# Kernel optimization log

Hardware: AMD Instinct MI355X
Metric: run time of the kernel (lower is better)

## Reference

```python
import jax, jax.numpy as jnp
import numpy as np

SEQ, B, I, H = 2048, 64, 512, 512

def setup_inputs() -> dict:
    key = jax.random.key(0)
    k1, k2, k3 = jax.random.split(key, 3)
    return {
        "input": jax.random.normal(k1, (SEQ, B, I), dtype=jnp.float32),
        "hx": jnp.zeros((1, B, H), dtype=jnp.float32),
        "weight_ih": jax.random.normal(k2, (H, I), dtype=jnp.float32) * 0.01,
        "weight_hh": jax.random.normal(k3, (H, H), dtype=jnp.float32) * 0.01,
        "bias_ih": jnp.zeros((H,), dtype=jnp.float32),
        "bias_hh": jnp.zeros((H,), dtype=jnp.float32),
    }

def reference(input, hx, weight_ih, weight_hh, bias_ih, bias_hh):
    # Batch the input-side projection across all timesteps in one GEMM:
    # [S,B,I] @ [I,H] -> [S,B,H]
    x_proj = jnp.einsum('sbi,hi->sbh', input, weight_ih) + bias_ih + bias_hh
    h0 = hx[0]  # [B,H]

    def step(h, xp_t):
        h_new = jnp.tanh(xp_t + h @ weight_hh.T)
        return h_new, h_new

    h_last, outputs = jax.lax.scan(step, h0, x_proj)
    return outputs, h_last[None]
```

## Files before the change

### kernel.cpp

```cpp
#include <hip/hip_runtime.h>
#include <stdint.h>

#define S_LEN 2048
#define B_SZ  64
#define I_SZ  512
#define H_SZ  512

typedef __attribute__((ext_vector_type(8))) short bf16x8;
typedef __attribute__((ext_vector_type(4))) float f32x4;

__device__ __forceinline__ uint16_t f2b(float x) {
    uint32_t u = __float_as_uint(x);
    uint32_t r = (u + 0x7fffu + ((u >> 16) & 1u)) >> 16;
    return (uint16_t)r;
}

__device__ __forceinline__ float tfun(float v) {
    float e = __expf(2.f * v);
    return 1.f - 2.f / (e + 1.f);
}

__global__ void cvt_weights_kernel(const float* __restrict__ wih,
                                   const float* __restrict__ whh,
                                   uint16_t* __restrict__ wihb,
                                   uint16_t* __restrict__ whhb) {
    int i = (blockIdx.x * blockDim.x + threadIdx.x) * 4;
    float4 a = *reinterpret_cast<const float4*>(wih + i);
    float4 b = *reinterpret_cast<const float4*>(whh + i);
    union { uint16_t u[4]; uint2 v; } pa, pb;
    pa.u[0] = f2b(a.x); pa.u[1] = f2b(a.y); pa.u[2] = f2b(a.z); pa.u[3] = f2b(a.w);
    pb.u[0] = f2b(b.x); pb.u[1] = f2b(b.y); pb.u[2] = f2b(b.z); pb.u[3] = f2b(b.w);
    *reinterpret_cast<uint2*>(wihb + i) = pa.v;
    *reinterpret_cast<uint2*>(whhb + i) = pb.v;
}

#define BM 128
#define BN 128
#define BK 32

__launch_bounds__(256)
__global__ void xproj_gemm_kernel(const float* __restrict__ inp,
                                  const uint16_t* __restrict__ wihb,
                                  const float* __restrict__ bih,
                                  const float* __restrict__ bhh,
                                  float* __restrict__ xp)
{
    __shared__ __align__(16) uint16_t Asm[2][BM * BK];
    __shared__ __align__(16) uint16_t Bsm[2][BN * BK];

    const int tid  = threadIdx.x;
    const int lane = tid & 63;
    const int w    = tid >> 6;
    const int wm   = (w >> 1) * 64;
    const int wn   = (w & 1) * 64;
    const int bid  = blockIdx.x;
    const int m0   = (bid >> 2) * BM;
    const int n0   = (bid & 3) * BN;

    const int srow  = tid >> 1;
    const int shalf = (tid & 1) * 16;

    float bsum[4];
#pragma unroll
    for (int nn = 0; nn < 4; ++nn) {
        int col = n0 + wn + nn * 16 + (lane & 15);
        bsum[nn] = bih[col] + bhh[col];
    }

    f32x4 acc[4][4];
#pragma unroll
    for (int mm = 0; mm < 4; ++mm)
#pragma unroll
        for (int nn = 0; nn < 4; ++nn)
            acc[mm][nn] = f32x4{0.f, 0.f, 0.f, 0.f};

    float4 ar[4];
    bf16x8 br[2];

    auto loadA = [&](int kt) {
        const float* g = inp + (size_t)(m0 + srow) * I_SZ + kt * BK + shalf;
#pragma unroll
        for (int q = 0; q < 4; ++q) ar[q] = *reinterpret_cast<const float4*>(g + q * 4);
    };
    auto loadB = [&](int kt) {
        const uint16_t* g = wihb + (size_t)(n0 + srow) * I_SZ + kt * BK + shalf;
        br[0] = *reinterpret_cast<const bf16x8*>(g);
        br[1] = *reinterpret_cast<const bf16x8*>(g + 8);
    };
    auto writeA = [&](int buf) {
        alignas(16) uint16_t tmp[16];
#pragma unroll
        for (int q = 0; q < 4; ++q) {
            tmp[q * 4 + 0] = f2b(ar[q].x); tmp[q * 4 + 1] = f2b(ar[q].y);
            tmp[q * 4 + 2] = f2b(ar[q].z); tmp[q * 4 + 3] = f2b(ar[q].w);
        }
        *reinterpret_cast<bf16x8*>(&Asm[buf][srow * BK + shalf])     = *reinterpret_cast<bf16x8*>(tmp);
        *reinterpret_cast<bf16x8*>(&Asm[buf][srow * BK + shalf + 8]) = *reinterpret_cast<bf16x8*>(tmp + 8);
    };
    auto writeB = [&](int buf) {
        *reinterpret_cast<bf16x8*>(&Bsm[buf][srow * BK + shalf])     = br[0];
        *reinterpret_cast<bf16x8*>(&Bsm[buf][srow * BK + shalf + 8]) = br[1];
    };

    loadA(0); loadB(0); writeA(0); writeB(0);
    __syncthreads();

    for (int kt = 0; kt < I_SZ / BK; ++kt) {
        const int cur = kt & 1;
        const bool more = (kt + 1) < I_SZ / BK;
        if (more) { loadA(kt + 1); loadB(kt + 1); }

        bf16x8 afrag[4], bfrag[4];
#pragma unroll
        for (int mm = 0; mm < 4; ++mm)
            afrag[mm] = *reinterpret_cast<const bf16x8*>(
                &Asm[cur][(wm + mm * 16 + (lane & 15)) * BK + (lane >> 4) * 8]);
#pragma unroll
        for (int nn = 0; nn < 4; ++nn)
            bfrag[nn] = *reinterpret_cast<const bf16x8*>(
                &Bsm[cur][(wn + nn * 16 + (lane & 15)) * BK + (lane >> 4) * 8]);
#pragma unroll
        for (int mm = 0; mm < 4; ++mm)
#pragma unroll
            for (int nn = 0; nn < 4; ++nn)
                acc[mm][nn] = __builtin_amdgcn_mfma_f32_16x16x32_bf16(
                    afrag[mm], bfrag[nn], acc[mm][nn], 0, 0, 0);

        if (more) { writeA(cur ^ 1); writeB(cur ^ 1); }
        __syncthreads();
    }

#pragma unroll
    for (int mm = 0; mm < 4; ++mm) {
        const int rbase = m0 + wm + mm * 16 + (lane >> 4) * 4;
#pragma unroll
        for (int nn = 0; nn < 4; ++nn) {
            const int col = n0 + wn + nn * 16 + (lane & 15);
#pragma unroll
            for (int r = 0; r < 4; ++r)
                xp[(size_t)(rbase + r) * H_SZ + col] = acc[mm][nn][r] + bsum[nn];
        }
    }
}


#define REP16(M) M(0) M(1) M(2) M(3) M(4) M(5) M(6) M(7) \
                 M(8) M(9) M(10) M(11) M(12) M(13) M(14) M(15)

#define LDW(jt, kt) (*reinterpret_cast<const bf16x8*>( \
    whhb + (size_t)(w * 64 + (jt) * 16 + r16) * H_SZ + (kt) * 32 + q * 8))

#define DECLA(k) bf16x8 rA##k, rB##k, rC##k;
#define LOADA(k) { \
    bf16x8 t0 = LDW(0, k), t1 = LDW(1, k), t2 = LDW(2, k); \
    asm("" : "=a"(rA##k) : "0"(t0)); \
    asm("" : "=a"(rB##k) : "0"(t1)); \
    asm("" : "=a"(rC##k) : "0"(t2)); }

#define KSTEP(k) { \
    bf16x8 bf = *reinterpret_cast<const bf16x8*>(hb + (k) * 32 + q * 8); \
    bf16x8 al = *reinterpret_cast<const bf16x8*>(&Asm[(w * 16 + (k)) * 512 + lane * 8]); \
    c0 = __builtin_amdgcn_mfma_f32_16x16x32_bf16(rA##k, bf, c0, 0, 0, 0); \
    c1 = __builtin_amdgcn_mfma_f32_16x16x32_bf16(rB##k, bf, c1, 0, 0, 0); \
    c2 = __builtin_amdgcn_mfma_f32_16x16x32_bf16(rC##k, bf, c2, 0, 0, 0); \
    c3 = __builtin_amdgcn_mfma_f32_16x16x32_bf16(al,   bf, c3, 0, 0, 0); }

#define STEP(P, XP, sidx, CHKLAST)                                                          \
  {                                                                                          \
    const uint16_t* hb = &hsm[P][0];                                                         \
    f32x4 c0{0.f,0.f,0.f,0.f}, c1{0.f,0.f,0.f,0.f}, c2{0.f,0.f,0.f,0.f}, c3{0.f,0.f,0.f,0.f};\
    REP16(KSTEP)                                                                             \
    if (r16 == 0) {                                                                          \
      *reinterpret_cast<f32x4*>(&ysm[w * 64 +  0 + q * 4]) = c0;                             \
      *reinterpret_cast<f32x4*>(&ysm[w * 64 + 16 + q * 4]) = c1;                             \
      *reinterpret_cast<f32x4*>(&ysm[w * 64 + 32 + q * 4]) = c2;                             \
      *reinterpret_cast<f32x4*>(&ysm[w * 64 + 48 + q * 4]) = c3;                             \
    }                                                                                        \
    asm volatile("s_waitcnt lgkmcnt(0)" ::: "memory");                                       \
    __builtin_amdgcn_s_barrier();                                                            \
    float th = tfun(ysm[tid] + XP);                                                          \
    out[((size_t)(sidx) * B_SZ + b) * H_SZ + tid] = th;                                      \
    hsm[(P) ^ 1][tid] = f2b(th);                                                             \
    if (CHKLAST && (sidx) == S_LEN - 1)                                                      \
      out[(size_t)S_LEN * B_SZ * H_SZ + (size_t)b * H_SZ + tid] = th;                        \
    { int prow = ((sidx) + 2 < S_LEN) ? ((sidx) + 2) : 0;                                    \
      XP = out[((size_t)prow * B_SZ + b) * H_SZ + tid]; }                                    \
    asm volatile("s_waitcnt lgkmcnt(0)" ::: "memory");                                       \
    __builtin_amdgcn_s_barrier();                                                            \
  }

__global__ __launch_bounds__(512)
__attribute__((amdgpu_waves_per_eu(2, 2)))
void rnn_rec_kernel(const uint16_t* __restrict__ whhb,
                    const float* __restrict__ hx,
                    float* __restrict__ out)
{
    __shared__ __align__(16) uint16_t Asm[8 * 16 * 512];
    __shared__ __align__(16) uint16_t hsm[2][512];
    __shared__ __align__(16) float    ysm[512];

    const int tid  = threadIdx.x;
    const int lane = tid & 63;
    const int w    = tid >> 6;
    const int b    = blockIdx.x;
    const int r16  = lane & 15;
    const int q    = lane >> 4;

    REP16(DECLA)
    REP16(LOADA)

#pragma unroll
    for (int kt = 0; kt < 16; ++kt)
        *reinterpret_cast<bf16x8*>(&Asm[(w * 16 + kt) * 512 + lane * 8]) =
            *reinterpret_cast<const bf16x8*>(
                whhb + (size_t)(w * 64 + 48 + r16) * H_SZ + kt * 32 + q * 8);

    hsm[0][tid] = f2b(hx[(size_t)b * H_SZ + tid]);

    float xpA = out[((size_t)0 * B_SZ + b) * H_SZ + tid];
    float xpB = out[((size_t)1 * B_SZ + b) * H_SZ + tid];
    __syncthreads();

    for (int s = 0; s < S_LEN; s += 2) {
        STEP(0, xpA, s, 0)
        STEP(1, xpB, s + 1, 1)
    }
}

extern "C" void kernel_launch(void* const* d_in, const int* in_sizes, int n_in,
                              void* d_out, int out_size, void* d_ws, size_t ws_size,
                              hipStream_t stream) {
    const float* inp = (const float*)d_in[0];
    const float* hx  = (const float*)d_in[1];
    const float* wih = (const float*)d_in[2];
    const float* whh = (const float*)d_in[3];
    const float* bih = (const float*)d_in[4];
    const float* bhh = (const float*)d_in[5];
    float* out = (float*)d_out;

    uint16_t* wihb = (uint16_t*)d_ws;
    uint16_t* whhb = wihb + (size_t)H_SZ * I_SZ;

    cvt_weights_kernel<<<256, 256, 0, stream>>>(wih, whh, wihb, whhb);

    const int grid_gemm = (S_LEN * B_SZ / BM) * (H_SZ / BN);
    xproj_gemm_kernel<<<grid_gemm, 256, 0, stream>>>(inp, wihb, bih, bhh, out);

    rnn_rec_kernel<<<B_SZ, 512, 0, stream>>>(whhb, hx, out);
}
```

Measured before the change: 3.221 ms.

## Keep more recurrent weights in AGPRs and issue MFMAs via inline asm

Moves 12 of the 16 k-tiles of the fourth weight column block from LDS into AGPRs, so only 4 k-tiles per wave are read from shared memory each step. The MFMA sequences are now emitted as inline assembly with hand-placed s_nop hazards, which cuts per-step LDS traffic and lets the compiler do less scheduling. In exchange it uses many more AGPRs, which risks spilling, and relies on the manually inserted nop counts being correct for MFMA dependency hazards.

```diff
diff --git a/kernel.cpp b/kernel.cpp
--- a/kernel.cpp
+++ b/kernel.cpp
@@ -146,30 +146,58 @@
 
 #define REP16(M) M(0) M(1) M(2) M(3) M(4) M(5) M(6) M(7) \
                  M(8) M(9) M(10) M(11) M(12) M(13) M(14) M(15)
+#define REP12(M) M(0) M(1) M(2) M(3) M(4) M(5) M(6) M(7) \
+                 M(8) M(9) M(10) M(11)
 
 #define LDW(jt, kt) (*reinterpret_cast<const bf16x8*>( \
     whhb + (size_t)(w * 64 + (jt) * 16 + r16) * H_SZ + (kt) * 32 + q * 8))
 
-#define DECLA(k) bf16x8 rA##k, rB##k, rC##k;
-#define LOADA(k) { \
+#define DECL3(k) bf16x8 rA##k, rB##k, rC##k;
+#define DECLD(k) bf16x8 rD##k;
+#define LOAD3(k) { \
     bf16x8 t0 = LDW(0, k), t1 = LDW(1, k), t2 = LDW(2, k); \
     asm("" : "=a"(rA##k) : "0"(t0)); \
     asm("" : "=a"(rB##k) : "0"(t1)); \
     asm("" : "=a"(rC##k) : "0"(t2)); }
-
-#define KSTEP(k) { \
-    bf16x8 bf = *reinterpret_cast<const bf16x8*>(hb + (k) * 32 + q * 8); \
-    bf16x8 al = *reinterpret_cast<const bf16x8*>(&Asm[(w * 16 + (k)) * 512 + lane * 8]); \
-    c0 = __builtin_amdgcn_mfma_f32_16x16x32_bf16(rA##k, bf, c0, 0, 0, 0); \
-    c1 = __builtin_amdgcn_mfma_f32_16x16x32_bf16(rB##k, bf, c1, 0, 0, 0); \
-    c2 = __builtin_amdgcn_mfma_f32_16x16x32_bf16(rC##k, bf, c2, 0, 0, 0); \
-    c3 = __builtin_amdgcn_mfma_f32_16x16x32_bf16(al,   bf, c3, 0, 0, 0); }
+#define LOADD(k) { \
+    bf16x8 t3 = LDW(3, k); \
+    asm("" : "=a"(rD##k) : "0"(t3)); }
+
+#define BF(k) (*reinterpret_cast<const bf16x8*>(hb + (k) * 32 + q * 8))
+#define AL(k) (*reinterpret_cast<const bf16x8*>(&WD[(w * 4 + (k) - 12) * 512 + lane * 8]))
+
+#define MFMA4 \
+    "v_mfma_f32_16x16x32_bf16 %0, %4, %8, %0\n\t" \
+    "v_mfma_f32_16x16x32_bf16 %1, %5, %8, %1\n\t" \
+    "v_mfma_f32_16x16x32_bf16 %2, %6, %8, %2\n\t" \
+    "v_mfma_f32_16x16x32_bf16 %3, %7, %8, %3"
+
+#define K_FIRST(k) { bf16x8 bf = BF(k); \
+    asm("s_nop 3\n\t" MFMA4 \
+        : "+v"(c0), "+v"(c1), "+v"(c2), "+v"(c3) \
+        : "a"(rA##k), "a"(rB##k), "a"(rC##k), "a"(rD##k), "v"(bf)); }
+#define K_AGPR(k) { bf16x8 bf = BF(k); \
+    asm(MFMA4 \
+        : "+v"(c0), "+v"(c1), "+v"(c2), "+v"(c3) \
+        : "a"(rA##k), "a"(rB##k), "a"(rC##k), "a"(rD##k), "v"(bf)); }
+#define K_LDS(k) { bf16x8 bf = BF(k); bf16x8 al = AL(k); \
+    asm(MFMA4 \
+        : "+v"(c0), "+v"(c1), "+v"(c2), "+v"(c3) \
+        : "a"(rA##k), "a"(rB##k), "a"(rC##k), "v"(al), "v"(bf)); }
+#define K_LAST(k) { bf16x8 bf = BF(k); bf16x8 al = AL(k); \
+    asm(MFMA4 "\n\ts_nop 7\n\ts_nop 7" \
+        : "+v"(c0), "+v"(c1), "+v"(c2), "+v"(c3) \
+        : "a"(rA##k), "a"(rB##k), "a"(rC##k), "v"(al), "v"(bf)); }
 
 #define STEP(P, XP, sidx, CHKLAST)                                                          \
   {                                                                                          \
     const uint16_t* hb = &hsm[P][0];                                                         \
     f32x4 c0{0.f,0.f,0.f,0.f}, c1{0.f,0.f,0.f,0.f}, c2{0.f,0.f,0.f,0.f}, c3{0.f,0.f,0.f,0.f};\
-    REP16(KSTEP)                                                                             \
+    K_FIRST(0)                                                                               \
+    K_AGPR(1) K_AGPR(2) K_AGPR(3) K_AGPR(4)  K_AGPR(5)  K_AGPR(6)                            \
+    K_AGPR(7) K_AGPR(8) K_AGPR(9) K_AGPR(10) K_AGPR(11)                                      \
+    K_LDS(12) K_LDS(13) K_LDS(14)                                                            \
+    K_LAST(15)                                                                               \
     if (r16 == 0) {                                                                          \
       *reinterpret_cast<f32x4*>(&ysm[w * 64 +  0 + q * 4]) = c0;                             \
       *reinterpret_cast<f32x4*>(&ysm[w * 64 + 16 + q * 4]) = c1;                             \
@@ -195,7 +223,7 @@
                     const float* __restrict__ hx,
                     float* __restrict__ out)
 {
-    __shared__ __align__(16) uint16_t Asm[8 * 16 * 512];
+    __shared__ __align__(16) uint16_t WD[8 * 4 * 512];
     __shared__ __align__(16) uint16_t hsm[2][512];
     __shared__ __align__(16) float    ysm[512];
 
@@ -206,14 +234,14 @@
     const int r16  = lane & 15;
     const int q    = lane >> 4;
 
-    REP16(DECLA)
-    REP16(LOADA)
-
-#pragma unroll
-    for (int kt = 0; kt < 16; ++kt)
-        *reinterpret_cast<bf16x8*>(&Asm[(w * 16 + kt) * 512 + lane * 8]) =
-            *reinterpret_cast<const bf16x8*>(
-                whhb + (size_t)(w * 64 + 48 + r16) * H_SZ + kt * 32 + q * 8);
+    REP16(DECL3)
+    REP12(DECLD)
+    REP16(LOAD3)
+    REP12(LOADD)
+
+#pragma unroll
+    for (int kt = 12; kt < 16; ++kt)
+        *reinterpret_cast<bf16x8*>(&WD[(w * 4 + kt - 12) * 512 + lane * 8]) = LDW(3, kt);
 
     hsm[0][tid] = f2b(hx[(size_t)b * H_SZ + tid]);
 
```

Result: slower. 7.475 ms (+132.1%).

## Convert W_ih inside GEMM and stream most of fourth W_hh tile from global

Applied to the files above, without the earlier changes.

The GEMM now loads fp32 W_ih directly and converts it to bf16 while staging into shared memory, so the conversion kernel only handles W_hh. In the recurrent kernel, the fourth 16-row weight tile per wave is held in LDS for only 4 of 16 k-steps; the other 12 are re-read from global (L2) every timestep. This cuts LDS use from 128KB to 32KB, which may ease occupancy or LDS pressure. In exchange it adds global-load latency on the serial recurrence critical path.

```diff
diff --git a/kernel.cpp b/kernel.cpp
--- a/kernel.cpp
+++ b/kernel.cpp
@@ -20,17 +20,12 @@
     return 1.f - 2.f / (e + 1.f);
 }
 
-__global__ void cvt_weights_kernel(const float* __restrict__ wih,
-                                   const float* __restrict__ whh,
-                                   uint16_t* __restrict__ wihb,
+__global__ void cvt_weights_kernel(const float* __restrict__ whh,
                                    uint16_t* __restrict__ whhb) {
     int i = (blockIdx.x * blockDim.x + threadIdx.x) * 4;
-    float4 a = *reinterpret_cast<const float4*>(wih + i);
     float4 b = *reinterpret_cast<const float4*>(whh + i);
-    union { uint16_t u[4]; uint2 v; } pa, pb;
-    pa.u[0] = f2b(a.x); pa.u[1] = f2b(a.y); pa.u[2] = f2b(a.z); pa.u[3] = f2b(a.w);
+    union { uint16_t u[4]; uint2 v; } pb;
     pb.u[0] = f2b(b.x); pb.u[1] = f2b(b.y); pb.u[2] = f2b(b.z); pb.u[3] = f2b(b.w);
-    *reinterpret_cast<uint2*>(wihb + i) = pa.v;
     *reinterpret_cast<uint2*>(whhb + i) = pb.v;
 }
 
@@ -40,7 +35,7 @@
 
 __launch_bounds__(256)
 __global__ void xproj_gemm_kernel(const float* __restrict__ inp,
-                                  const uint16_t* __restrict__ wihb,
+                                  const float* __restrict__ wih,
                                   const float* __restrict__ bih,
                                   const float* __restrict__ bhh,
                                   float* __restrict__ xp)
@@ -74,8 +69,7 @@
         for (int nn = 0; nn < 4; ++nn)
             acc[mm][nn] = f32x4{0.f, 0.f, 0.f, 0.f};
 
-    float4 ar[4];
-    bf16x8 br[2];
+    float4 ar[4], br[4];
 
     auto loadA = [&](int kt) {
         const float* g = inp + (size_t)(m0 + srow) * I_SZ + kt * BK + shalf;
@@ -83,24 +77,22 @@
         for (int q = 0; q < 4; ++q) ar[q] = *reinterpret_cast<const float4*>(g + q * 4);
     };
     auto loadB = [&](int kt) {
-        const uint16_t* g = wihb + (size_t)(n0 + srow) * I_SZ + kt * BK + shalf;
-        br[0] = *reinterpret_cast<const bf16x8*>(g);
-        br[1] = *reinterpret_cast<const bf16x8*>(g + 8);
+        const float* g = wih + (size_t)(n0 + srow) * I_SZ + kt * BK + shalf;
+#pragma unroll
+        for (int q = 0; q < 4; ++q) br[q] = *reinterpret_cast<const float4*>(g + q * 4);
     };
-    auto writeA = [&](int buf) {
+    auto cvt16 = [&](float4* src, uint16_t* dst) {
         alignas(16) uint16_t tmp[16];
 #pragma unroll
         for (int q = 0; q < 4; ++q) {
-            tmp[q * 4 + 0] = f2b(ar[q].x); tmp[q * 4 + 1] = f2b(ar[q].y);
-            tmp[q * 4 + 2] = f2b(ar[q].z); tmp[q * 4 + 3] = f2b(ar[q].w);
+            tmp[q * 4 + 0] = f2b(src[q].x); tmp[q * 4 + 1] = f2b(src[q].y);
+            tmp[q * 4 + 2] = f2b(src[q].z); tmp[q * 4 + 3] = f2b(src[q].w);
         }
-        *reinterpret_cast<bf16x8*>(&Asm[buf][srow * BK + shalf])     = *reinterpret_cast<bf16x8*>(tmp);
-        *reinterpret_cast<bf16x8*>(&Asm[buf][srow * BK + shalf + 8]) = *reinterpret_cast<bf16x8*>(tmp + 8);
+        *reinterpret_cast<bf16x8*>(dst)     = *reinterpret_cast<bf16x8*>(tmp);
+        *reinterpret_cast<bf16x8*>(dst + 8) = *reinterpret_cast<bf16x8*>(tmp + 8);
     };
-    auto writeB = [&](int buf) {
-        *reinterpret_cast<bf16x8*>(&Bsm[buf][srow * BK + shalf])     = br[0];
-        *reinterpret_cast<bf16x8*>(&Bsm[buf][srow * BK + shalf + 8]) = br[1];
-    };
+    auto writeA = [&](int buf) { cvt16(ar, &Asm[buf][srow * BK + shalf]); };
+    auto writeB = [&](int buf) { cvt16(br, &Bsm[buf][srow * BK + shalf]); };
 
     loadA(0); loadB(0); writeA(0); writeB(0);
     __syncthreads();
@@ -150,26 +142,34 @@
 #define LDW(jt, kt) (*reinterpret_cast<const bf16x8*>( \
     whhb + (size_t)(w * 64 + (jt) * 16 + r16) * H_SZ + (kt) * 32 + q * 8))
 
-#define DECLA(k) bf16x8 rA##k, rB##k, rC##k;
-#define LOADA(k) { \
+#define DECL3(k) bf16x8 rA##k, rB##k, rC##k;
+#define LOAD3(k) { \
     bf16x8 t0 = LDW(0, k), t1 = LDW(1, k), t2 = LDW(2, k); \
     asm("" : "=a"(rA##k) : "0"(t0)); \
     asm("" : "=a"(rB##k) : "0"(t1)); \
     asm("" : "=a"(rC##k) : "0"(t2)); }
 
-#define KSTEP(k) { \
+#define MFMA_B(A, B, C) __builtin_amdgcn_mfma_f32_16x16x32_bf16((A), (B), (C), 0, 0, 0)
+
+#define KSTEP_L(k) { \
     bf16x8 bf = *reinterpret_cast<const bf16x8*>(hb + (k) * 32 + q * 8); \
-    bf16x8 al = *reinterpret_cast<const bf16x8*>(&Asm[(w * 16 + (k)) * 512 + lane * 8]); \
-    c0 = __builtin_amdgcn_mfma_f32_16x16x32_bf16(rA##k, bf, c0, 0, 0, 0); \
-    c1 = __builtin_amdgcn_mfma_f32_16x16x32_bf16(rB##k, bf, c1, 0, 0, 0); \
-    c2 = __builtin_amdgcn_mfma_f32_16x16x32_bf16(rC##k, bf, c2, 0, 0, 0); \
-    c3 = __builtin_amdgcn_mfma_f32_16x16x32_bf16(al,   bf, c3, 0, 0, 0); }
+    bf16x8 al = *reinterpret_cast<const bf16x8*>(&WD[(w * 4 + (k)) * 512 + lane * 8]); \
+    c0 = MFMA_B(rA##k, bf, c0); c1 = MFMA_B(rB##k, bf, c1); \
+    c2 = MFMA_B(rC##k, bf, c2); c3 = MFMA_B(al,    bf, c3); }
+#define KSTEP_G(k) { \
+    bf16x8 bf = *reinterpret_cast<const bf16x8*>(hb + (k) * 32 + q * 8); \
+    bf16x8 dl = LDW(3, k); \
+    c0 = MFMA_B(rA##k, bf, c0); c1 = MFMA_B(rB##k, bf, c1); \
+    c2 = MFMA_B(rC##k, bf, c2); c3 = MFMA_B(dl,    bf, c3); }
 
 #define STEP(P, XP, sidx, CHKLAST)                                                          \
   {                                                                                          \
     const uint16_t* hb = &hsm[P][0];                                                         \
     f32x4 c0{0.f,0.f,0.f,0.f}, c1{0.f,0.f,0.f,0.f}, c2{0.f,0.f,0.f,0.f}, c3{0.f,0.f,0.f,0.f};\
-    REP16(KSTEP)                                                                             \
+    KSTEP_L(0)  KSTEP_L(1)  KSTEP_L(2)  KSTEP_L(3)                                           \
+    KSTEP_G(4)  KSTEP_G(5)  KSTEP_G(6)  KSTEP_G(7)                                           \
+    KSTEP_G(8)  KSTEP_G(9)  KSTEP_G(10) KSTEP_G(11)                                          \
+    KSTEP_G(12) KSTEP_G(13) KSTEP_G(14) KSTEP_G(15)                                          \
     if (r16 == 0) {                                                                          \
       *reinterpret_cast<f32x4*>(&ysm[w * 64 +  0 + q * 4]) = c0;                             \
       *reinterpret_cast<f32x4*>(&ysm[w * 64 + 16 + q * 4]) = c1;                             \
@@ -195,7 +195,7 @@
                     const float* __restrict__ hx,
                     float* __restrict__ out)
 {
-    __shared__ __align__(16) uint16_t Asm[8 * 16 * 512];
+    __shared__ __align__(16) uint16_t WD[8 * 4 * 512];
     __shared__ __align__(16) uint16_t hsm[2][512];
     __shared__ __align__(16) float    ysm[512];
 
@@ -206,14 +206,12 @@
     const int r16  = lane & 15;
     const int q    = lane >> 4;
 
-    REP16(DECLA)
-    REP16(LOADA)
-
-#pragma unroll
-    for (int kt = 0; kt < 16; ++kt)
-        *reinterpret_cast<bf16x8*>(&Asm[(w * 16 + kt) * 512 + lane * 8]) =
-            *reinterpret_cast<const bf16x8*>(
-                whhb + (size_t)(w * 64 + 48 + r16) * H_SZ + kt * 32 + q * 8);
+    REP16(DECL3)
+    REP16(LOAD3)
+
+#pragma unroll
+    for (int kt = 0; kt < 4; ++kt)
+        *reinterpret_cast<bf16x8*>(&WD[(w * 4 + kt) * 512 + lane * 8]) = LDW(3, kt);
 
     hsm[0][tid] = f2b(hx[(size_t)b * H_SZ + tid]);
 
@@ -238,13 +236,12 @@
     const float* bhh = (const float*)d_in[5];
     float* out = (float*)d_out;
 
-    uint16_t* wihb = (uint16_t*)d_ws;
-    uint16_t* whhb = wihb + (size_t)H_SZ * I_SZ;
-
-    cvt_weights_kernel<<<256, 256, 0, stream>>>(wih, whh, wihb, whhb);
+    uint16_t* whhb = (uint16_t*)d_ws;
+
+    cvt_weights_kernel<<<256, 256, 0, stream>>>(whh, whhb);
 
     const int grid_gemm = (S_LEN * B_SZ / BM) * (H_SZ / BN);
-    xproj_gemm_kernel<<<grid_gemm, 256, 0, stream>>>(inp, wihb, bih, bhh, out);
+    xproj_gemm_kernel<<<grid_gemm, 256, 0, stream>>>(inp, wih, bih, bhh, out);
 
     rnn_rec_kernel<<<B_SZ, 512, 0, stream>>>(whhb, hx, out);
 }
```

After: 5.617 ms. 1.74x slower.
